# Optimization experiments

Hardware: AMD Instinct MI355X
Metric: run time of the kernel (lower is better)

## Reference

```python
import jax, jax.numpy as jnp
import numpy as np

VOCAB, E, H, L, N = 32000, 256, 512, 512, 64


def setup_inputs() -> dict:
    key = jax.random.key(0)
    ks = jax.random.split(key, 8)
    s_in = 1.0 / np.sqrt(H + E)
    return {
        "x": jax.random.randint(ks[0], (L, N), 0, VOCAB),
        "emb": jax.random.normal(ks[1], (VOCAB, E), dtype=jnp.float32),
        # weights stored (in, out); math identical to torch Linear with W.T
        "Wz": jax.random.uniform(ks[2], (H + E, H), jnp.float32, -s_in, s_in),
        "bz": jax.random.uniform(ks[3], (H,), jnp.float32, -s_in, s_in),
        "Wr": jax.random.uniform(ks[4], (H + E, H), jnp.float32, -s_in, s_in),
        "br": jax.random.uniform(ks[5], (H,), jnp.float32, -s_in, s_in),
        "Wh": jax.random.uniform(ks[6], (H + E, H), jnp.float32, -s_in, s_in),
        "bh": jax.random.uniform(ks[7], (H,), jnp.float32, -s_in, s_in),
    }


def reference(x, emb, Wz, bz, Wr, br, Wh, bh):
    # x: (L, N) int indices -> embedded once: (L, N, E)
    xe = emb[x]
    h0 = jnp.zeros((x.shape[1], Wz.shape[1]), dtype=emb.dtype)

    def step(h, e_t):
        hx = jnp.concatenate([h, e_t], axis=1)            # (N, H+E)
        z = jax.nn.sigmoid(hx @ Wz + bz)                  # update gate
        r = jax.nn.sigmoid(hx @ Wr + br)                  # reset gate
        rhx = jnp.concatenate([r * h, e_t], axis=1)
        h_tilde = jnp.tanh(rhx @ Wh + bh)
        h_new = (1.0 - z) * h + z * h_tilde
        return h_new, h_new

    _, hs = jax.lax.scan(step, h0, xe)                    # hs: (L, N, H)
    return hs
```

## Files before the change

kernel.cpp:

```cpp
#include <hip/hip_runtime.h>


#define LSTEPS 512
#define NBATCH 64
#define HDIM   512
#define EDIM   256
#define KDIM   768
#define NWORK  16
#define COLS   32
#define TPB    256
#define NLAUNCH 128
#define FASTBUDGET 300

typedef _Float16 f16x8 __attribute__((ext_vector_type(8)));
typedef float    f32x4 __attribute__((ext_vector_type(4)));
typedef unsigned long long u64;

#define MFMA __builtin_amdgcn_mfma_f32_16x16x32_f16

__device__ __forceinline__ float sigm(float x){ return 1.0f/(1.0f+__expf(-x)); }
__device__ __forceinline__ float tanh_fast(float x){
  float e = __expf(2.0f*x);
  return 1.0f - 2.0f/(e + 1.0f);
}
__device__ __forceinline__ unsigned f16b(float x){
  union { _Float16 h; unsigned short u; } c; c.h = (_Float16)x; return (unsigned)c.u;
}
__device__ __forceinline__ f16x8 AFU(u64 a, u64 b){
  union { u64 d[2]; f16x8 v; } c; c.d[0] = a; c.d[1] = b; return c.v;
}

__device__ __forceinline__ unsigned ld_sc0_u32(const unsigned* a){
  unsigned r;
  asm volatile("global_load_dword %0, %1, off sc0\n\ts_waitcnt vmcnt(0)"
               : "=v"(r) : "v"(a) : "memory");
  return r;
}

__global__ void prep_w(const float* __restrict__ Wz, const float* __restrict__ Wr,
                       const float* __restrict__ Wh, _Float16* __restrict__ wbuf){
  int tid = blockIdx.x*256 + threadIdx.x;
  int g   = tid / (HDIM*KDIM);
  int rem = tid - g*(HDIM*KDIM);
  int j   = rem / KDIM;
  int k   = rem - j*KDIM;
  const float* W = (g==0) ? Wz : ((g==1) ? Wr : Wh);
  wbuf[tid] = (_Float16)W[(size_t)k*HDIM + j];
}

__global__ void prep_emb(const int* __restrict__ x, const float* __restrict__ emb,
                         _Float16* __restrict__ ebuf){
  int tid = blockIdx.x*256 + threadIdx.x;
  int k4  = tid & 63;
  int tn  = tid >> 6;
  int row = x[tn];
  const float4 v = *(const float4*)(emb + (size_t)row*EDIM + (k4<<2));
  union { _Float16 h[4]; uint2 u; } p;
  p.h[0] = (_Float16)v.x; p.h[1] = (_Float16)v.y;
  p.h[2] = (_Float16)v.z; p.h[3] = (_Float16)v.w;
  *(uint2*)(ebuf + (size_t)tn*EDIM + (k4<<2)) = p.u;
}

__device__ __forceinline__ void pack2(int lane, float v0, float v1, float v2,
                                      float v3, unsigned* w0, unsigned* w1, int* r0){
  unsigned p01 = f16b(v0) | (f16b(v1) << 16);
  unsigned p23 = f16b(v2) | (f16b(v3) << 16);
  unsigned q01 = __shfl_xor(p01, 1, 64);
  unsigned q23 = __shfl_xor(p23, 1, 64);
  if (lane & 1){
    *w0 = (q23 & 0xffffu) | (p23 << 16);
    *w1 = (q23 >> 16)     | (p23 & 0xffff0000u);
    *r0 = 2;
  } else {
    *w0 = (p01 & 0xffffu) | (q01 << 16);
    *w1 = (p01 >> 16)     | (q01 & 0xffff0000u);
    *r0 = 0;
  }
}

__device__ __forceinline__ void store_dual(_Float16* bufL2, _Float16* bufM,
                                           int jc2, int n0, int lane,
                                           float v0, float v1, float v2, float v3){
  unsigned w0, w1; int rr;
  pack2(lane, v0, v1, v2, v3, &w0, &w1, &rr);
  int r0 = n0 + rr;
  *(unsigned*)(bufL2 + (size_t)r0*HDIM + jc2)     = w0;
  *(unsigned*)(bufL2 + (size_t)(r0+1)*HDIM + jc2) = w1;
  __hip_atomic_store((unsigned*)(bufM + (size_t)r0*HDIM + jc2),     w0,
                     __ATOMIC_RELAXED, __HIP_MEMORY_SCOPE_AGENT);
  __hip_atomic_store((unsigned*)(bufM + (size_t)(r0+1)*HDIM + jc2), w1,
                     __ATOMIC_RELAXED, __HIP_MEMORY_SCOPE_AGENT);
}

__device__ __forceinline__ int waitx(const unsigned* flL2, const unsigned* flM,
                                     unsigned target, int fpd){
  const int l15 = threadIdx.x & 15;
  if (!fpd){
    for (int i = 0; i < FASTBUDGET; ++i){
      unsigned v = ld_sc0_u32(flL2 + l15);
      if (__all((int)(v >= target))) return 0;
    }
  }
  for (;;){
    unsigned v = __hip_atomic_load(flM + l15, __ATOMIC_RELAXED,
                                   __HIP_MEMORY_SCOPE_AGENT);
    if (__all((int)(v >= target))) break;
  }
  return 1;
}

__global__ __launch_bounds__(TPB, 1) void gru_persist(
    const _Float16* __restrict__ wbuf,
    const _Float16* __restrict__ ebuf,
    const float* __restrict__ bz, const float* __restrict__ br, const float* __restrict__ bh,
    _Float16* __restrict__ hxL, _Float16* __restrict__ hxM,
    _Float16* __restrict__ rhL, _Float16* __restrict__ rhM,
    unsigned* __restrict__ hflL, unsigned* __restrict__ hflM,
    unsigned* __restrict__ rflL, unsigned* __restrict__ rflM,
    unsigned* __restrict__ xcnt, unsigned* __restrict__ winner,
    float* __restrict__ out)
{
  __shared__ char wlds[3*COLS*1536];
  __shared__ int s_slot;

  if (threadIdx.x == 0){
    unsigned xcd;
    asm volatile("s_getreg_b32 %0, hwreg(HW_REG_XCC_ID)" : "=s"(xcd));
    xcd &= 7;
    unsigned rank = __hip_atomic_fetch_add(&xcnt[xcd], 1u,
                        __ATOMIC_RELAXED, __HIP_MEMORY_SCOPE_AGENT);
    int slot = -1;
    if (rank < NWORK){
      if (rank == NWORK-1){
        unsigned exp = 0u;
        __hip_atomic_compare_exchange_strong(winner, &exp, xcd+1u,
            __ATOMIC_RELAXED, __ATOMIC_RELAXED, __HIP_MEMORY_SCOPE_AGENT);
      }
      unsigned w;
      do { w = __hip_atomic_load(winner, __ATOMIC_RELAXED,
                                 __HIP_MEMORY_SCOPE_AGENT); }
      while (w == 0u);
      if (w == xcd+1u) slot = (int)rank;
    }
    s_slot = slot;
  }
  __syncthreads();
  const int slot = s_slot;
  if (slot < 0) return;

  const int jbase = slot * COLS;
  for (int cidx = threadIdx.x; cidx < 3*COLS*96; cidx += TPB){
    int g   = cidx / (COLS*96);
    int rem = cidx - g*(COLS*96);
    int col = rem / 96;
    int kch = rem - col*96;
    const uint4 v = *(const uint4*)(wbuf + ((size_t)(g*HDIM + jbase + col))*KDIM + kch*8);
    int off = (((g*COLS + col)*1536) + kch*16) ^ ((col & 7) << 4);
    *(uint4*)(wlds + off) = v;
  }
  __syncthreads();

  const int lane = threadIdx.x & 63;
  const int wave = threadIdx.x >> 6;
  const int c15  = lane & 15;
  const int kgrp = lane >> 4;
  const int arow = wave*16 + c15;
  const int n0   = wave*16 + kgrp*4;
  const int swz  = (c15 & 7) << 4;
  const int jcol0 = jbase + c15;
  const int jcol1 = jbase + 16 + c15;
  const int jc20  = jcol0 & ~1;
  const int jc21  = jcol1 & ~1;
  const int lz0 = ((0*COLS + c15     )*1536) + kgrp*16;
  const int lz1 = ((0*COLS + c15 + 16)*1536) + kgrp*16;
  const int lr0 = ((1*COLS + c15     )*1536) + kgrp*16;
  const int lr1 = ((1*COLS + c15 + 16)*1536) + kgrp*16;
  const int lh0 = ((2*COLS + c15     )*1536) + kgrp*16;
  const int lh1 = ((2*COLS + c15 + 16)*1536) + kgrp*16;
  const float bzj0 = bz[jcol0], bzj1 = bz[jcol1];
  const float brj0 = br[jcol0], brj1 = br[jcol1];
  const float bhj0 = bh[jcol0], bhj1 = bh[jcol1];
  const u64* hrowL = (const u64*)hxL + (size_t)arow*128 + kgrp*2;
  const u64* hrowM = (const u64*)hxM + (size_t)arow*128 + kgrp*2;
  const u64* rrowL = (const u64*)rhL + (size_t)arow*128 + kgrp*2;
  const u64* rrowM = (const u64*)rhM + (size_t)arow*128 + kgrp*2;
  unsigned* myhflL = hflL + wave*NWORK;
  unsigned* myhflM = hflM + wave*NWORK;
  unsigned* myrflL = rflL + wave*NWORK;
  unsigned* myrflM = rflM + wave*NWORK;
  float hreg0[4] = {0,0,0,0}, hreg1[4] = {0,0,0,0};
  int fpd = 0;

  u64 q[32];
  f16x8 aereg[8];

#define LOADQ_FAST(BASE) do {                                                 \
    asm volatile("buffer_inv" ::: "memory");                                  \
    _Pragma("unroll")                                                         \
    for (int kc = 0; kc < 16; ++kc){                                          \
      q[2*kc]   = (BASE)[kc*8];                                               \
      q[2*kc+1] = (BASE)[kc*8 + 1];                                           \
    }                                                                         \
  } while (0)

#define LOADQ_MALL(BASE) do {                                                 \
    _Pragma("unroll")                                                         \
    for (int kc = 0; kc < 16; ++kc){                                          \
      q[2*kc]   = __hip_atomic_load((BASE) + kc*8,     __ATOMIC_RELAXED,      \
                                    __HIP_MEMORY_SCOPE_AGENT);                \
      q[2*kc+1] = __hip_atomic_load((BASE) + kc*8 + 1, __ATOMIC_RELAXED,      \
                                    __HIP_MEMORY_SCOPE_AGENT);                \
    }                                                                         \
  } while (0)

  {
    const _Float16* ae0 = ebuf + (size_t)arow*EDIM + kgrp*8;
    #pragma unroll
    for (int kc = 0; kc < 8; ++kc) aereg[kc] = *(const f16x8*)(ae0 + kc*32);
  }

  for (int t = 0; t < LSTEPS; ++t){
    const unsigned tagn = (unsigned)(t + 1);

    f32x4 accr0 = {0,0,0,0}, accr1 = {0,0,0,0};
    #pragma unroll
    for (int kc = 0; kc < 8; ++kc){
      f16x8 b0 = *(const f16x8*)(wlds + ((lr0 + (16+kc)*64) ^ swz));
      f16x8 b1 = *(const f16x8*)(wlds + ((lr1 + (16+kc)*64) ^ swz));
      accr0 = MFMA(aereg[kc], b0, accr0, 0, 0, 0);
      accr1 = MFMA(aereg[kc], b1, accr1, 0, 0, 0);
    }
    {
      int fb = waitx(myhflL, myhflM, (unsigned)t, fpd);
      fpd |= fb;
      if (fb) LOADQ_MALL(hrowM); else LOADQ_FAST(hrowL);
    }
    #pragma unroll
    for (int kc = 0; kc < 16; ++kc){
      f16x8 a  = AFU(q[2*kc], q[2*kc+1]);
      f16x8 b0 = *(const f16x8*)(wlds + ((lr0 + kc*64) ^ swz));
      f16x8 b1 = *(const f16x8*)(wlds + ((lr1 + kc*64) ^ swz));
      accr0 = MFMA(a, b0, accr0, 0, 0, 0);
      accr1 = MFMA(a, b1, accr1, 0, 0, 0);
    }
    float rh0[4], rh1[4];
    #pragma unroll
    for (int i = 0; i < 4; ++i){
      rh0[i] = sigm(accr0[i] + brj0) * hreg0[i];
      rh1[i] = sigm(accr1[i] + brj1) * hreg1[i];
    }
    store_dual(rhL, rhM, jc20, n0, lane, rh0[0], rh0[1], rh0[2], rh0[3]);
    store_dual(rhL, rhM, jc21, n0, lane, rh1[0], rh1[1], rh1[2], rh1[3]);
    asm volatile("s_waitcnt vmcnt(0)" ::: "memory");
    __builtin_amdgcn_sched_barrier(0);
    if (lane == 0){
      *(volatile unsigned*)&myrflL[slot] = tagn;
      __hip_atomic_store(&myrflM[slot], tagn,
                         __ATOMIC_RELAXED, __HIP_MEMORY_SCOPE_AGENT);
    }

    f32x4 accz0 = {0,0,0,0}, accz1 = {0,0,0,0};
    f32x4 acch0 = {0,0,0,0}, acch1 = {0,0,0,0};
    #pragma unroll
    for (int kc = 0; kc < 16; ++kc){
      f16x8 a  = AFU(q[2*kc], q[2*kc+1]);
      f16x8 b0 = *(const f16x8*)(wlds + ((lz0 + kc*64) ^ swz));
      f16x8 b1 = *(const f16x8*)(wlds + ((lz1 + kc*64) ^ swz));
      accz0 = MFMA(a, b0, accz0, 0, 0, 0);
      accz1 = MFMA(a, b1, accz1, 0, 0, 0);
    }
    #pragma unroll
    for (int kc = 0; kc < 8; ++kc){
      f16x8 z0 = *(const f16x8*)(wlds + ((lz0 + (16+kc)*64) ^ swz));
      f16x8 z1 = *(const f16x8*)(wlds + ((lz1 + (16+kc)*64) ^ swz));
      f16x8 h0 = *(const f16x8*)(wlds + ((lh0 + (16+kc)*64) ^ swz));
      f16x8 h1 = *(const f16x8*)(wlds + ((lh1 + (16+kc)*64) ^ swz));
      accz0 = MFMA(aereg[kc], z0, accz0, 0, 0, 0);
      accz1 = MFMA(aereg[kc], z1, accz1, 0, 0, 0);
      acch0 = MFMA(aereg[kc], h0, acch0, 0, 0, 0);
      acch1 = MFMA(aereg[kc], h1, acch1, 0, 0, 0);
    }
    float zreg0[4], zreg1[4];
    #pragma unroll
    for (int i = 0; i < 4; ++i){
      zreg0[i] = sigm(accz0[i] + bzj0);
      zreg1[i] = sigm(accz1[i] + bzj1);
    }

    {
      int fb = waitx(myrflL, myrflM, tagn, fpd);
      fpd |= fb;
      if (fb) LOADQ_MALL(rrowM); else LOADQ_FAST(rrowL);
    }
    #pragma unroll
    for (int kc = 0; kc < 16; ++kc){
      f16x8 a  = AFU(q[2*kc], q[2*kc+1]);
      f16x8 b0 = *(const f16x8*)(wlds + ((lh0 + kc*64) ^ swz));
      f16x8 b1 = *(const f16x8*)(wlds + ((lh1 + kc*64) ^ swz));
      acch0 = MFMA(a, b0, acch0, 0, 0, 0);
      acch1 = MFMA(a, b1, acch1, 0, 0, 0);
    }
    #pragma unroll
    for (int i = 0; i < 4; ++i){
      float ht0 = tanh_fast(acch0[i] + bhj0);
      float ht1 = tanh_fast(acch1[i] + bhj1);
      hreg0[i] = hreg0[i] + zreg0[i]*(ht0 - hreg0[i]);
      hreg1[i] = hreg1[i] + zreg1[i]*(ht1 - hreg1[i]);
    }
    store_dual(hxL, hxM, jc20, n0, lane, hreg0[0], hreg0[1], hreg0[2], hreg0[3]);
    store_dual(hxL, hxM, jc21, n0, lane, hreg1[0], hreg1[1], hreg1[2], hreg1[3]);
    asm volatile("s_waitcnt vmcnt(0)" ::: "memory");
    __builtin_amdgcn_sched_barrier(0);
    if (lane == 0){
      *(volatile unsigned*)&myhflL[slot] = tagn;
      __hip_atomic_store(&myhflM[slot], tagn,
                         __ATOMIC_RELAXED, __HIP_MEMORY_SCOPE_AGENT);
    }

    #pragma unroll
    for (int i = 0; i < 4; ++i){
      int n = n0 + i;
      out[((size_t)t*NBATCH + n)*HDIM + jcol0] = hreg0[i];
      out[((size_t)t*NBATCH + n)*HDIM + jcol1] = hreg1[i];
    }
    if (t + 1 < LSTEPS){
      const _Float16* aen = ebuf + ((size_t)(t+1)*NBATCH + arow)*EDIM + kgrp*8;
      #pragma unroll
      for (int kc = 0; kc < 8; ++kc) aereg[kc] = *(const f16x8*)(aen + kc*32);
    }
  }
#undef LOADQ_FAST
#undef LOADQ_MALL
}

extern "C" void kernel_launch(void* const* d_in, const int* in_sizes, int n_in,
                              void* d_out, int out_size, void* d_ws, size_t ws_size,
                              hipStream_t stream) {
  const int*   x   = (const int*)  d_in[0];
  const float* emb = (const float*)d_in[1];
  const float* Wz  = (const float*)d_in[2];
  const float* bz  = (const float*)d_in[3];
  const float* Wr  = (const float*)d_in[4];
  const float* br  = (const float*)d_in[5];
  const float* Wh  = (const float*)d_in[6];
  const float* bh  = (const float*)d_in[7];
  float* out = (float*)d_out;
  char*  ws  = (char*)d_ws;

  size_t off = 0;
  unsigned* xcnt   = (unsigned*)(ws + off); off += 64;
  unsigned* winner = (unsigned*)(ws + off); off += 64;
  unsigned* hflL = (unsigned*)(ws + off); off += 4*NWORK*4;
  unsigned* hflM = (unsigned*)(ws + off); off += 4*NWORK*4;
  unsigned* rflL = (unsigned*)(ws + off); off += 4*NWORK*4;
  unsigned* rflM = (unsigned*)(ws + off); off += 4*NWORK*4;
  _Float16* hxL  = (_Float16*)(ws + off); off += (size_t)NBATCH*HDIM*2;
  _Float16* hxM  = (_Float16*)(ws + off); off += (size_t)NBATCH*HDIM*2;
  size_t zero_bytes = off;
  _Float16* rhL  = (_Float16*)(ws + off); off += (size_t)NBATCH*HDIM*2;
  _Float16* rhM  = (_Float16*)(ws + off); off += (size_t)NBATCH*HDIM*2;
  _Float16* wbuf = (_Float16*)(ws + off); off += (size_t)3*HDIM*KDIM*2;
  _Float16* ebuf = (_Float16*)(ws + off); off += (size_t)LSTEPS*NBATCH*EDIM*2;

  hipMemsetAsync(ws, 0, zero_bytes, stream);

  prep_w  <<<(3*HDIM*KDIM)/256,          256, 0, stream>>>(Wz, Wr, Wh, wbuf);
  prep_emb<<<(LSTEPS*NBATCH*EDIM/4)/256, 256, 0, stream>>>(x, emb, ebuf);
  gru_persist<<<NLAUNCH, TPB, 0, stream>>>(wbuf, ebuf, bz, br, bh,
                                           hxL, hxM, rhL, rhM,
                                           hflL, hflM, rflL, rflM,
                                           xcnt, winner, out);
}
```

Before: 5.921 ms.

## Publish L2 ready flags before MALL stores and prefetch next-step embeddings early

Each step now raises the fast L2 flag as soon as the L2 copies of r*h and h are drained. The matching MALL data stores and MALL flag updates are deferred until just before the next wait, taking them off the critical cross-workgroup handoff. The next timestep's embedding fragment is loaded into a second register buffer mid-step instead of at the end of the step. The fast-path spin budget is also raised before falling back to MALL polling. This adds register pressure from the extra embedding buffer and more draining points, and makes the flag protocol more intricate.

```diff
diff --git a/kernel.cpp b/kernel.cpp
--- a/kernel.cpp
+++ b/kernel.cpp
@@ -10,13 +10,15 @@
 #define COLS   32
 #define TPB    256
 #define NLAUNCH 128
-#define FASTBUDGET 300
+#define FASTBUDGET 2000
 
 typedef _Float16 f16x8 __attribute__((ext_vector_type(8)));
 typedef float    f32x4 __attribute__((ext_vector_type(4)));
 typedef unsigned long long u64;
 
 #define MFMA __builtin_amdgcn_mfma_f32_16x16x32_f16
+#define VMDRAIN() do { asm volatile("s_waitcnt vmcnt(0)" ::: "memory"); \
+                       __builtin_amdgcn_sched_barrier(0); } while (0)
 
 __device__ __forceinline__ float sigm(float x){ return 1.0f/(1.0f+__expf(-x)); }
 __device__ __forceinline__ float tanh_fast(float x){
@@ -62,7 +64,7 @@
 }
 
 __device__ __forceinline__ void pack2(int lane, float v0, float v1, float v2,
-                                      float v3, unsigned* w0, unsigned* w1, int* r0){
+                                      float v3, unsigned* w0, unsigned* w1, int* rr){
   unsigned p01 = f16b(v0) | (f16b(v1) << 16);
   unsigned p23 = f16b(v2) | (f16b(v3) << 16);
   unsigned q01 = __shfl_xor(p01, 1, 64);
@@ -70,26 +72,12 @@
   if (lane & 1){
     *w0 = (q23 & 0xffffu) | (p23 << 16);
     *w1 = (q23 >> 16)     | (p23 & 0xffff0000u);
-    *r0 = 2;
+    *rr = 2;
   } else {
     *w0 = (p01 & 0xffffu) | (q01 << 16);
     *w1 = (p01 >> 16)     | (q01 & 0xffff0000u);
-    *r0 = 0;
-  }
-}
-
-__device__ __forceinline__ void store_dual(_Float16* bufL2, _Float16* bufM,
-                                           int jc2, int n0, int lane,
-                                           float v0, float v1, float v2, float v3){
-  unsigned w0, w1; int rr;
-  pack2(lane, v0, v1, v2, v3, &w0, &w1, &rr);
-  int r0 = n0 + rr;
-  *(unsigned*)(bufL2 + (size_t)r0*HDIM + jc2)     = w0;
-  *(unsigned*)(bufL2 + (size_t)(r0+1)*HDIM + jc2) = w1;
-  __hip_atomic_store((unsigned*)(bufM + (size_t)r0*HDIM + jc2),     w0,
-                     __ATOMIC_RELAXED, __HIP_MEMORY_SCOPE_AGENT);
-  __hip_atomic_store((unsigned*)(bufM + (size_t)(r0+1)*HDIM + jc2), w1,
-                     __ATOMIC_RELAXED, __HIP_MEMORY_SCOPE_AGENT);
+    *rr = 0;
+  }
 }
 
 __device__ __forceinline__ int waitx(const unsigned* flL2, const unsigned* flM,
@@ -192,7 +180,7 @@
   int fpd = 0;
 
   u64 q[32];
-  f16x8 aereg[8];
+  f16x8 aeA[8], aeB[8];
 
 #define LOADQ_FAST(BASE) do {                                                 \
     asm volatile("buffer_inv" ::: "memory");                                  \
@@ -216,7 +204,7 @@
   {
     const _Float16* ae0 = ebuf + (size_t)arow*EDIM + kgrp*8;
     #pragma unroll
-    for (int kc = 0; kc < 8; ++kc) aereg[kc] = *(const f16x8*)(ae0 + kc*32);
+    for (int kc = 0; kc < 8; ++kc) aeA[kc] = *(const f16x8*)(ae0 + kc*32);
   }
 
   for (int t = 0; t < LSTEPS; ++t){
@@ -227,9 +215,13 @@
     for (int kc = 0; kc < 8; ++kc){
       f16x8 b0 = *(const f16x8*)(wlds + ((lr0 + (16+kc)*64) ^ swz));
       f16x8 b1 = *(const f16x8*)(wlds + ((lr1 + (16+kc)*64) ^ swz));
-      accr0 = MFMA(aereg[kc], b0, accr0, 0, 0, 0);
-      accr1 = MFMA(aereg[kc], b1, accr1, 0, 0, 0);
-    }
+      accr0 = MFMA(aeA[kc], b0, accr0, 0, 0, 0);
+      accr1 = MFMA(aeA[kc], b1, accr1, 0, 0, 0);
+    }
+    VMDRAIN();
+    if (lane == 0)
+      __hip_atomic_store(&myhflM[slot], (unsigned)t,
+                         __ATOMIC_RELAXED, __HIP_MEMORY_SCOPE_AGENT);
     {
       int fb = waitx(myhflL, myhflM, (unsigned)t, fpd);
       fpd |= fb;
@@ -243,20 +235,37 @@
       accr0 = MFMA(a, b0, accr0, 0, 0, 0);
       accr1 = MFMA(a, b1, accr1, 0, 0, 0);
     }
-    float rh0[4], rh1[4];
-    #pragma unroll
-    for (int i = 0; i < 4; ++i){
-      rh0[i] = sigm(accr0[i] + brj0) * hreg0[i];
-      rh1[i] = sigm(accr1[i] + brj1) * hreg1[i];
-    }
-    store_dual(rhL, rhM, jc20, n0, lane, rh0[0], rh0[1], rh0[2], rh0[3]);
-    store_dual(rhL, rhM, jc21, n0, lane, rh1[0], rh1[1], rh1[2], rh1[3]);
-    asm volatile("s_waitcnt vmcnt(0)" ::: "memory");
-    __builtin_amdgcn_sched_barrier(0);
-    if (lane == 0){
-      *(volatile unsigned*)&myrflL[slot] = tagn;
-      __hip_atomic_store(&myrflM[slot], tagn,
-                         __ATOMIC_RELAXED, __HIP_MEMORY_SCOPE_AGENT);
+    unsigned w00, w01, w10, w11; int rr;
+    {
+      float rh0[4], rh1[4];
+      #pragma unroll
+      for (int i = 0; i < 4; ++i){
+        rh0[i] = sigm(accr0[i] + brj0) * hreg0[i];
+        rh1[i] = sigm(accr1[i] + brj1) * hreg1[i];
+      }
+      pack2(lane, rh0[0], rh0[1], rh0[2], rh0[3], &w00, &w01, &rr);
+      pack2(lane, rh1[0], rh1[1], rh1[2], rh1[3], &w10, &w11, &rr);
+    }
+    const int r0 = n0 + rr;
+    *(unsigned*)(rhL + (size_t)r0*HDIM + jc20)     = w00;
+    *(unsigned*)(rhL + (size_t)(r0+1)*HDIM + jc20) = w01;
+    *(unsigned*)(rhL + (size_t)r0*HDIM + jc21)     = w10;
+    *(unsigned*)(rhL + (size_t)(r0+1)*HDIM + jc21) = w11;
+    VMDRAIN();
+    if (lane == 0) *(volatile unsigned*)&myrflL[slot] = tagn;
+    __hip_atomic_store((unsigned*)(rhM + (size_t)r0*HDIM + jc20),     w00,
+                       __ATOMIC_RELAXED, __HIP_MEMORY_SCOPE_AGENT);
+    __hip_atomic_store((unsigned*)(rhM + (size_t)(r0+1)*HDIM + jc20), w01,
+                       __ATOMIC_RELAXED, __HIP_MEMORY_SCOPE_AGENT);
+    __hip_atomic_store((unsigned*)(rhM + (size_t)r0*HDIM + jc21),     w10,
+                       __ATOMIC_RELAXED, __HIP_MEMORY_SCOPE_AGENT);
+    __hip_atomic_store((unsigned*)(rhM + (size_t)(r0+1)*HDIM + jc21), w11,
+                       __ATOMIC_RELAXED, __HIP_MEMORY_SCOPE_AGENT);
+    {
+      const int tn = (t + 1 < LSTEPS) ? (t + 1) : t;
+      const _Float16* aen = ebuf + ((size_t)tn*NBATCH + arow)*EDIM + kgrp*8;
+      #pragma unroll
+      for (int kc = 0; kc < 8; ++kc) aeB[kc] = *(const f16x8*)(aen + kc*32);
     }
 
     f32x4 accz0 = {0,0,0,0}, accz1 = {0,0,0,0};
@@ -275,10 +284,10 @@
       f16x8 z1 = *(const f16x8*)(wlds + ((lz1 + (16+kc)*64) ^ swz));
       f16x8 h0 = *(const f16x8*)(wlds + ((lh0 + (16+kc)*64) ^ swz));
       f16x8 h1 = *(const f16x8*)(wlds + ((lh1 + (16+kc)*64) ^ swz));
-      accz0 = MFMA(aereg[kc], z0, accz0, 0, 0, 0);
-      accz1 = MFMA(aereg[kc], z1, accz1, 0, 0, 0);
-      acch0 = MFMA(aereg[kc], h0, acch0, 0, 0, 0);
-      acch1 = MFMA(aereg[kc], h1, acch1, 0, 0, 0);
+      accz0 = MFMA(aeA[kc], z0, accz0, 0, 0, 0);
+      accz1 = MFMA(aeA[kc], z1, accz1, 0, 0, 0);
+      acch0 = MFMA(aeA[kc], h0, acch0, 0, 0, 0);
+      acch1 = MFMA(aeA[kc], h1, acch1, 0, 0, 0);
     }
     float zreg0[4], zreg1[4];
     #pragma unroll
@@ -287,6 +296,10 @@
       zreg1[i] = sigm(accz1[i] + bzj1);
     }
 
+    VMDRAIN();
+    if (lane == 0)
+      __hip_atomic_store(&myrflM[slot], tagn,
+                         __ATOMIC_RELAXED, __HIP_MEMORY_SCOPE_AGENT);
     {
       int fb = waitx(myrflL, myrflM, tagn, fpd);
       fpd |= fb;
@@ -307,30 +320,35 @@
       hreg0[i] = hreg0[i] + zreg0[i]*(ht0 - hreg0[i]);
       hreg1[i] = hreg1[i] + zreg1[i]*(ht1 - hreg1[i]);
     }
-    store_dual(hxL, hxM, jc20, n0, lane, hreg0[0], hreg0[1], hreg0[2], hreg0[3]);
-    store_dual(hxL, hxM, jc21, n0, lane, hreg1[0], hreg1[1], hreg1[2], hreg1[3]);
-    asm volatile("s_waitcnt vmcnt(0)" ::: "memory");
-    __builtin_amdgcn_sched_barrier(0);
-    if (lane == 0){
-      *(volatile unsigned*)&myhflL[slot] = tagn;
-      __hip_atomic_store(&myhflM[slot], tagn,
-                         __ATOMIC_RELAXED, __HIP_MEMORY_SCOPE_AGENT);
-    }
-
+    {
+      unsigned v00, v01, v10, v11; int rr2;
+      pack2(lane, hreg0[0], hreg0[1], hreg0[2], hreg0[3], &v00, &v01, &rr2);
+      pack2(lane, hreg1[0], hreg1[1], hreg1[2], hreg1[3], &v10, &v11, &rr2);
+      const int s0 = n0 + rr2;
+      *(unsigned*)(hxL + (size_t)s0*HDIM + jc20)     = v00;
+      *(unsigned*)(hxL + (size_t)(s0+1)*HDIM + jc20) = v01;
+      *(unsigned*)(hxL + (size_t)s0*HDIM + jc21)     = v10;
+      *(unsigned*)(hxL + (size_t)(s0+1)*HDIM + jc21) = v11;
+      VMDRAIN();
+      if (lane == 0) *(volatile unsigned*)&myhflL[slot] = tagn;
+      __hip_atomic_store((unsigned*)(hxM + (size_t)s0*HDIM + jc20),     v00,
+                         __ATOMIC_RELAXED, __HIP_MEMORY_SCOPE_AGENT);
+      __hip_atomic_store((unsigned*)(hxM + (size_t)(s0+1)*HDIM + jc20), v01,
+                         __ATOMIC_RELAXED, __HIP_MEMORY_SCOPE_AGENT);
+      __hip_atomic_store((unsigned*)(hxM + (size_t)s0*HDIM + jc21),     v10,
+                         __ATOMIC_RELAXED, __HIP_MEMORY_SCOPE_AGENT);
+      __hip_atomic_store((unsigned*)(hxM + (size_t)(s0+1)*HDIM + jc21), v11,
+                         __ATOMIC_RELAXED, __HIP_MEMORY_SCOPE_AGENT);
+    }
     #pragma unroll
     for (int i = 0; i < 4; ++i){
       int n = n0 + i;
       out[((size_t)t*NBATCH + n)*HDIM + jcol0] = hreg0[i];
       out[((size_t)t*NBATCH + n)*HDIM + jcol1] = hreg1[i];
     }
-    if (t + 1 < LSTEPS){
-      const _Float16* aen = ebuf + ((size_t)(t+1)*NBATCH + arow)*EDIM + kgrp*8;
-      #pragma unroll
-      for (int kc = 0; kc < 8; ++kc) aereg[kc] = *(const f16x8*)(aen + kc*32);
-    }
-  }
-#undef LOADQ_FAST
-#undef LOADQ_MALL
+    #pragma unroll
+    for (int kc = 0; kc < 8; ++kc) aeA[kc] = aeB[kc];
+  }
 }
 
 extern "C" void kernel_launch(void* const* d_in, const int* in_sizes, int n_in,
```

Result: slower. 6.607 ms (+11.6%).
